# Optimization experiments

Measured on AMD Instinct MI355X. Metric: run time of the kernel, lower is better.

## Reference

```python
import jax, jax.numpy as jnp
import numpy as np

KS = 3
K3 = KS ** 3
NUM_K = 4
KM_ITERS = 10  # fixed Lloyd iterations (original runs to tolerance)


def _unfold3d(xp, d, h, w):
    # xp: [B, C, d+2, h+2, w+2] -> [B, C, d, h, w, 27]; kernel dims flattened as (k1,k2,k3)
    sl = [xp[:, :, i:i + d, j:j + h, l:l + w]
          for i in range(KS) for j in range(KS) for l in range(KS)]
    return jnp.stack(sl, axis=-1)


def _kmeans(pts):
    # pts: [N, C]. Deterministic init with first NUM_K points, fixed Lloyd iterations.
    cent0 = pts[:NUM_K]

    def assign(cent):
        d2 = (jnp.sum(pts * pts, -1, keepdims=True)
              - 2.0 * (pts @ cent.T) + jnp.sum(cent * cent, -1))  # [N, K]
        return jnp.argmin(d2, axis=-1)

    def step(cent, _):
        oh = jax.nn.one_hot(assign(cent), NUM_K, dtype=pts.dtype)  # [N, K]
        cnt = jnp.maximum(oh.sum(0), 1.0)
        cent = (oh.T @ pts) / cnt[:, None]
        return cent, None

    cent, _ = jax.lax.scan(step, cent0, None, length=KM_ITERS)
    return assign(cent), cent


def _mlp3(z, w1, b1, w2, b2, w3, b3):
    z = jax.nn.relu(z @ w1 + b1)
    z = jax.nn.relu(z @ w2 + b2)
    return z @ w3 + b3


def reference(x, proj_w, base_w, gk_w1, gk_b1, gk_w2, gk_b2, gk_w3, gk_b3,
              gb_w1, gb_b1, gb_w2, gb_b2, gb_w3, gb_b3, prelu_a):
    b, c, d, h, w = x.shape
    o = base_w.shape[0]
    n = d * h * w
    x_in = x
    # 1x1x1 input projection (no bias)
    xp = jnp.einsum('oi,bidhw->bodhw', proj_w, x)
    xp = jnp.pad(xp, ((0, 0), (0, 0), (1, 1), (1, 1), (1, 1)))
    patches = _unfold3d(xp, d, h, w)                                # [b,c,d,h,w,27]
    # mean_type 's': mean over kernel dims -> per-voxel channel summary
    x_mean = patches.mean(-1).reshape(b, c, n).transpose(0, 2, 1)   # [b,n,c]
    idx, cent = jax.vmap(_kmeans)(x_mean)                           # [b,n], [b,K,c]
    feat = cent.reshape(b, NUM_K * c)
    # per-cluster dynamic kernel gates in (0,1)
    w_i = jax.nn.sigmoid(_mlp3(feat, gk_w1, gk_b1, gk_w2, gk_b2, gk_w3, gk_b3))
    w_i = w_i.reshape(b, NUM_K, K3).transpose(1, 0, 2)[:, :, None, None, :]  # [K,b,1,1,27]
    weight = (w_i * base_w).reshape(NUM_K, b, o, c * K3)            # [K,b,o,c*27]
    bias = _mlp3(feat, gb_w1, gb_b1, gb_w2, gb_b2, gb_w3, gb_b3)
    bias = bias.reshape(b, NUM_K, o).transpose(1, 0, 2)[..., None]  # [K,b,o,1]
    # im2col: [b, c*27, n] with (c, k) channel-major flattening as in the torch rearrange
    xf = patches.reshape(b, c, n, K3).transpose(0, 1, 3, 2).reshape(b, c * K3, n)
    out = jnp.einsum('kbof,bfn->kbon', weight, xf) + bias           # [K,b,o,n]
    mask = jax.nn.one_hot(idx, NUM_K, dtype=out.dtype)              # [b,n,K]
    out = (out * mask.transpose(2, 0, 1)[:, :, None, :]).sum(0)     # [b,o,n]
    out = out.reshape(b, o, d, h, w)
    out = jnp.where(out >= 0, out, prelu_a * out)                   # PReLU (single param)
    return out + x_in


def setup_inputs():
    key = jax.random.key(0)
    ks = jax.random.split(key, 12)
    B, C, O, D = 1, 64, 64, 40
    inner, inner2 = 128, 64
    fin = C * NUM_K

    def lin(k, i, o_):
        s = 1.0 / np.sqrt(i)
        return jax.random.uniform(k, (i, o_), jnp.float32, -s, s)

    return {
        'x': jax.random.normal(ks[0], (B, C, D, D, D), jnp.float32),
        'proj_w': jax.random.normal(ks[1], (C, C), jnp.float32) / np.sqrt(C),
        'base_w': jax.random.normal(ks[2], (O, C, K3), jnp.float32) / np.sqrt(C * K3),
        'gk_w1': lin(ks[3], fin, inner), 'gk_b1': jnp.zeros((inner,), jnp.float32),
        'gk_w2': lin(ks[4], inner, inner), 'gk_b2': jnp.zeros((inner,), jnp.float32),
        'gk_w3': lin(ks[5], inner, K3 * NUM_K), 'gk_b3': jnp.zeros((K3 * NUM_K,), jnp.float32),
        'gb_w1': lin(ks[6], fin, inner2), 'gb_b1': jnp.zeros((inner2,), jnp.float32),
        'gb_w2': lin(ks[7], inner2, inner2), 'gb_b2': jnp.zeros((inner2,), jnp.float32),
        'gb_w3': lin(ks[8], inner2, O * NUM_K), 'gb_b3': jnp.zeros((O * NUM_K,), jnp.float32),
        'prelu_a': jnp.full((1,), 0.25, jnp.float32),
    }
```

## Files before the change

### kernel.cpp

```cpp
#include <hip/hip_runtime.h>
#include <math.h>

typedef short v8s __attribute__((ext_vector_type(8)));
typedef float v4f __attribute__((ext_vector_type(4)));

#define NVOX 64000
#define NPAD 74088
#define P2   1764
#define GSTR 592704
#define NCPY 32
#define ITST (NCPY*260)

__device__ __forceinline__ unsigned short bf16rne(float f){
  unsigned int u = __float_as_uint(f);
  u += 0x7FFFu + ((u >> 16) & 1u);
  return (unsigned short)(u >> 16);
}

__global__ __launch_bounds__(256) void prep_k(const float* __restrict__ x,
                                              const float* __restrict__ pw,
                                              float* __restrict__ xp,
                                              short* __restrict__ xpt,
                                              const float* __restrict__ bw,
                                              short* __restrict__ bwb){
  int tid = threadIdx.x;
  int bid = blockIdx.x;
  if (bid < 1000){
    int m = (bid >> 2) * 256 + tid;
    int quarter = bid & 3;
    float xv[64];
#pragma unroll
    for (int i = 0; i < 64; i++) xv[i] = x[(size_t)i * NVOX + m];
    int d = m / 1600; int r = m - d * 1600; int h = r / 40; int w = r - h * 40;
    int p = ((d + 1) * 42 + (h + 1)) * 42 + (w + 1);
    const float4* pw4 = (const float4*)pw;
    for (int g8 = quarter * 2; g8 < quarter * 2 + 2; g8++){
      v8s pk;
#pragma unroll
      for (int j = 0; j < 8; j++){
        int co = g8 * 8 + j;
        float acc = 0.f;
#pragma unroll
        for (int q = 0; q < 16; q++){
          float4 pv = pw4[co * 16 + q];
          acc = fmaf(pv.x, xv[4*q+0], acc);
          acc = fmaf(pv.y, xv[4*q+1], acc);
          acc = fmaf(pv.z, xv[4*q+2], acc);
          acc = fmaf(pv.w, xv[4*q+3], acc);
        }
        xp[(size_t)co * NVOX + m] = acc;
        pk[j] = (short)bf16rne(acc);
      }
      *(v8s*)(xpt + (size_t)g8 * GSTR + (size_t)p * 8) = pk;
    }
  } else if (bid < 1432){
    int e = (bid - 1000) * 256 + tid;
    int t5 = e >> 12; int rem = e & 4095;
    int o = rem >> 6; int c = rem & 63;
    bwb[e] = (short)bf16rne(bw[(o * 64 + c) * 27 + t5]);
  } else {
    v8s z = (v8s){0,0,0,0,0,0,0,0};
    for (int p = (bid - 1432) * 256 + tid; p < NPAD; p += 40 * 256){
      int d = p / P2; int rem = p - d * P2; int h = rem / 42; int w = rem - h * 42;
      if (d == 0 || d == 41 || h == 0 || h == 41 || w == 0 || w == 41){
#pragma unroll
        for (int g = 0; g < 8; g++)
          *(v8s*)(xpt + (size_t)g * GSTR + (size_t)p * 8) = z;
      }
    }
  }
}

__global__ __launch_bounds__(256) void boxwh_k(const float* __restrict__ in,
                                               float* __restrict__ out){
  __shared__ float s0[1600], s1[1600];
  size_t base = (size_t)blockIdx.x * 1600;
  int t = threadIdx.x;
  for (int e = t; e < 1600; e += 256) s0[e] = in[base + e];
  __syncthreads();
  for (int e = t; e < 1600; e += 256){
    int w = e % 40;
    float s = s0[e];
    if (w > 0)  s += s0[e - 1];
    if (w < 39) s += s0[e + 1];
    s1[e] = s;
  }
  __syncthreads();
  for (int e = t; e < 1600; e += 256){
    int h = e / 40;
    float s = s1[e];
    if (h > 0)  s += s1[e - 40];
    if (h < 39) s += s1[e + 40];
    out[base + e] = s;
  }
}
__global__ void boxd_k(const float* __restrict__ in, float* __restrict__ out){
  int g = blockIdx.x * 256 + threadIdx.x;
  int d = (g / 1600) % 40;
  float s = in[g];
  if (d > 0)  s += in[g - 1600];
  if (d < 39) s += in[g + 1600];
  out[g] = s * (1.f / 27.f);
}

__global__ __launch_bounds__(256) void transp_k(const float* __restrict__ in,
                                                float* __restrict__ out,
                                                float* __restrict__ km){
  __shared__ float tile[64][65];
  int t = threadIdx.x;
  int nb = blockIdx.x * 64;
  int l = t & 63, g = t >> 6;
  for (int j = 260 + blockIdx.x * 256 + t; j < 11 * ITST; j += 1000 * 256)
    km[j] = 0.f;
  for (int cc = g; cc < 64; cc += 4)
    tile[cc][l] = in[(size_t)cc * NVOX + nb + l];
  __syncthreads();
  if (blockIdx.x == 0){
    km[t] = tile[t & 63][t >> 6];
    if (t < 4) km[256 + t] = 1.f;
  }
  for (int nn = g; nn < 64; nn += 4)
    out[(size_t)(nb + nn) * 64 + l] = tile[l][nn];
}

__global__ __launch_bounds__(256) void assign_k(const float* __restrict__ xmt,
                                                const float* __restrict__ kin,
                                                float* __restrict__ kout,
                                                int* __restrict__ idx, int mode,
                      const float* __restrict__ w1, const float* __restrict__ b1,
                      const float* __restrict__ w2, const float* __restrict__ b2,
                      const float* __restrict__ w3, const float* __restrict__ b3,
                      const float* __restrict__ u1, const float* __restrict__ c1,
                      const float* __restrict__ u2, const float* __restrict__ c2,
                      const float* __restrict__ u3, const float* __restrict__ c3,
                      float* __restrict__ wi, float* __restrict__ bias){
  __shared__ float s_cent[256];
  __shared__ float s_cc[4];
  __shared__ float s_red[260];
  __shared__ float s_x[256 * 65];
  __shared__ int   s_kb[256];
  __shared__ float s_h1[128], s_h2[128], s_g1[64], s_g2[64];
  int t = threadIdx.x, lane = t & 63, wv = t >> 6;
  int n = blockIdx.x * 256 + t;
  {
    float sum = 0.f, cnt = 0.f;
#pragma unroll
    for (int s = 0; s < NCPY; s++){
      sum += kin[s * 260 + t];
      cnt += kin[s * 260 + 256 + (t >> 6)];
    }
    s_cent[t] = sum / fmaxf(cnt, 1.f);
  }
  for (int j = t; j < 260; j += 256) s_red[j] = 0.f;
  __syncthreads();
  if (t < 4){
    const float4* cc4 = (const float4*)(s_cent + t * 64);
    float s = 0.f;
#pragma unroll
    for (int q = 0; q < 16; q++){
      float4 v = cc4[q];
      s = fmaf(v.x, v.x, s); s = fmaf(v.y, v.y, s);
      s = fmaf(v.z, v.z, s); s = fmaf(v.w, v.w, s);
    }
    s_cc[t] = s;
  }
  __syncthreads();
  const float4* xt = (const float4*)(xmt + (size_t)n * 64);
  float4 xq[16];
#pragma unroll
  for (int q = 0; q < 16; q++) xq[q] = xt[q];
  float d0 = 0.f, d1 = 0.f, d2 = 0.f, d3 = 0.f;
  const float4* c4 = (const float4*)s_cent;
#pragma unroll
  for (int q = 0; q < 16; q++){
    float4 p0 = c4[q], p1 = c4[16 + q], p2 = c4[32 + q], p3 = c4[48 + q];
    d0 = fmaf(p0.x, xq[q].x, d0); d0 = fmaf(p0.y, xq[q].y, d0);
    d0 = fmaf(p0.z, xq[q].z, d0); d0 = fmaf(p0.w, xq[q].w, d0);
    d1 = fmaf(p1.x, xq[q].x, d1); d1 = fmaf(p1.y, xq[q].y, d1);
    d1 = fmaf(p1.z, xq[q].z, d1); d1 = fmaf(p1.w, xq[q].w, d1);
    d2 = fmaf(p2.x, xq[q].x, d2); d2 = fmaf(p2.y, xq[q].y, d2);
    d2 = fmaf(p2.z, xq[q].z, d2); d2 = fmaf(p2.w, xq[q].w, d2);
    d3 = fmaf(p3.x, xq[q].x, d3); d3 = fmaf(p3.y, xq[q].y, d3);
    d3 = fmaf(p3.z, xq[q].z, d3); d3 = fmaf(p3.w, xq[q].w, d3);
  }
  float sc0 = s_cc[0] - 2.f * d0;
  float sc1 = s_cc[1] - 2.f * d1;
  float sc2 = s_cc[2] - 2.f * d2;
  float sc3 = s_cc[3] - 2.f * d3;
  int kb = 0; float bs = sc0;
  if (sc1 < bs){ bs = sc1; kb = 1; }
  if (sc2 < bs){ bs = sc2; kb = 2; }
  if (sc3 < bs){ bs = sc3; kb = 3; }
  if (mode){
    idx[n] = kb;
    if (blockIdx.x == 0){
      __syncthreads();
      if (t < 128){
        float z = b1[t];
        for (int i = 0; i < 256; i++) z = fmaf(s_cent[i], w1[i * 128 + t], z);
        s_h1[t] = fmaxf(z, 0.f);
      }
      if (t < 64){
        float z = c1[t];
        for (int i = 0; i < 256; i++) z = fmaf(s_cent[i], u1[i * 64 + t], z);
        s_g1[t] = fmaxf(z, 0.f);
      }
      __syncthreads();
      if (t < 128){
        float z = b2[t];
        for (int i = 0; i < 128; i++) z = fmaf(s_h1[i], w2[i * 128 + t], z);
        s_h2[t] = fmaxf(z, 0.f);
      }
      if (t < 64){
        float z = c2[t];
        for (int i = 0; i < 64; i++) z = fmaf(s_g1[i], u2[i * 64 + t], z);
        s_g2[t] = fmaxf(z, 0.f);
      }
      __syncthreads();
      if (t < 108){
        float z = b3[t];
        for (int i = 0; i < 128; i++) z = fmaf(s_h2[i], w3[i * 108 + t], z);
        wi[t] = 1.f / (1.f + expf(-z));
      }
      {
        float z = c3[t];
        for (int i = 0; i < 64; i++) z = fmaf(s_g2[i], u3[i * 256 + t], z);
        bias[t] = z;
      }
    }
    return;
  }
  s_kb[t] = kb;
#pragma unroll
  for (int q = 0; q < 16; q++){
    s_x[t * 65 + 4*q + 0] = xq[q].x;
    s_x[t * 65 + 4*q + 1] = xq[q].y;
    s_x[t * 65 + 4*q + 2] = xq[q].z;
    s_x[t * 65 + 4*q + 3] = xq[q].w;
  }
  __syncthreads();
  float a0 = 0.f, a1 = 0.f, a2 = 0.f, a3 = 0.f;
  int rowbase = wv * 64;
#pragma unroll 16
  for (int j = 0; j < 64; j++){
    float v = s_x[(rowbase + j) * 65 + lane];
    int kj = s_kb[rowbase + j];
    a0 += (kj == 0) ? v : 0.f;
    a1 += (kj == 1) ? v : 0.f;
    a2 += (kj == 2) ? v : 0.f;
    a3 += (kj == 3) ? v : 0.f;
  }
  atomicAdd(&s_red[lane], a0);
  atomicAdd(&s_red[64 + lane], a1);
  atomicAdd(&s_red[128 + lane], a2);
  atomicAdd(&s_red[192 + lane], a3);
#pragma unroll
  for (int kk = 0; kk < 4; kk++){
    unsigned long long m = __ballot(kb == kk);
    if (lane == 0) atomicAdd(&s_red[256 + kk], (float)__popcll(m));
  }
  __syncthreads();
  float* kslot = kout + (blockIdx.x & (NCPY - 1)) * 260;
  for (int j = t; j < 260; j += 256) atomicAdd(&kslot[j], s_red[j]);
}

__global__ __launch_bounds__(256) void conv_k(const short* __restrict__ xpt,
                                              const short* __restrict__ bwb,
                                              const float* __restrict__ wi,
                                              const float* __restrict__ bias,
                                              const int* __restrict__ idx,
                                              const float* __restrict__ x,
                                              const float* __restrict__ pa,
                                              float* __restrict__ out){
  static const int POFF[27] = {
    -P2-42-1, -P2-42, -P2-42+1, -P2-1, -P2, -P2+1, -P2+42-1, -P2+42, -P2+42+1,
    -42-1, -42, -42+1, -1, 0, 1, 42-1, 42, 42+1,
    P2-42-1, P2-42, P2-42+1, P2-1, P2, P2+1, P2+42-1, P2+42, P2+42+1 };
  __shared__ float s_wi[108];
  __shared__ float s_bias[256];
  __shared__ float s_acc[64 * 68];
  int tid = threadIdx.x;
  for (int j = tid; j < 108; j += 256) s_wi[j] = wi[j];
  s_bias[tid] = bias[tid];
  __syncthreads();
  int wv = tid >> 6, lane = tid & 63;
  int kc = wv & 1, mh = wv >> 1;
  int col = lane & 15, kg = lane >> 4;
  int vb = blockIdx.x * 64;
  int p4[4], ki4[4];
#pragma unroll
  for (int nt = 0; nt < 4; nt++){
    int v = vb + nt * 16 + col;
    ki4[nt] = idx[v];
    int d = v / 1600; int r = v - d * 1600; int h = r / 40; int w = r - h * 40;
    p4[nt] = ((d + 1) * 42 + (h + 1)) * 42 + (w + 1);
  }
  const short* bg = xpt + (size_t)(kc * 4 + kg) * GSTR;
  const short* bp0 = bg + (size_t)p4[0] * 8;
  const short* bp1 = bg + (size_t)p4[1] * 8;
  const short* bp2 = bg + (size_t)p4[2] * 8;
  const short* bp3 = bg + (size_t)p4[3] * 8;
  int ao0 = (mh * 32 + col) * 64 + kc * 32 + kg * 8;
  int ao1 = ao0 + 16 * 64;
  v4f acc[2][4];
#pragma unroll
  for (int m2 = 0; m2 < 2; m2++)
#pragma unroll
    for (int nt = 0; nt < 4; nt++) acc[m2][nt] = (v4f){0.f, 0.f, 0.f, 0.f};
  v4f zero = {0.f, 0.f, 0.f, 0.f};
#pragma unroll 9
  for (int t = 0; t < 27; t++){
    int po8 = POFF[t] * 8;
    v8s a0 = *(const v8s*)(bwb + t * 4096 + ao0);
    v8s a1 = *(const v8s*)(bwb + t * 4096 + ao1);
    v8s b0 = *(const v8s*)(bp0 + po8);
    v8s b1 = *(const v8s*)(bp1 + po8);
    v8s b2 = *(const v8s*)(bp2 + po8);
    v8s b3 = *(const v8s*)(bp3 + po8);
    float wk0 = s_wi[ki4[0] * 27 + t];
    float wk1 = s_wi[ki4[1] * 27 + t];
    float wk2 = s_wi[ki4[2] * 27 + t];
    float wk3 = s_wi[ki4[3] * 27 + t];
    v4f tp;
    tp = __builtin_amdgcn_mfma_f32_16x16x32_bf16(a0, b0, zero, 0, 0, 0); acc[0][0] += tp * wk0;
    tp = __builtin_amdgcn_mfma_f32_16x16x32_bf16(a1, b0, zero, 0, 0, 0); acc[1][0] += tp * wk0;
    tp = __builtin_amdgcn_mfma_f32_16x16x32_bf16(a0, b1, zero, 0, 0, 0); acc[0][1] += tp * wk1;
    tp = __builtin_amdgcn_mfma_f32_16x16x32_bf16(a1, b1, zero, 0, 0, 0); acc[1][1] += tp * wk1;
    tp = __builtin_amdgcn_mfma_f32_16x16x32_bf16(a0, b2, zero, 0, 0, 0); acc[0][2] += tp * wk2;
    tp = __builtin_amdgcn_mfma_f32_16x16x32_bf16(a1, b2, zero, 0, 0, 0); acc[1][2] += tp * wk2;
    tp = __builtin_amdgcn_mfma_f32_16x16x32_bf16(a0, b3, zero, 0, 0, 0); acc[0][3] += tp * wk3;
    tp = __builtin_amdgcn_mfma_f32_16x16x32_bf16(a1, b3, zero, 0, 0, 0); acc[1][3] += tp * wk3;
  }
  __syncthreads();
  if (kc == 1){
#pragma unroll
    for (int m2 = 0; m2 < 2; m2++)
#pragma unroll
      for (int nt = 0; nt < 4; nt++)
        *(v4f*)(&s_acc[(nt * 16 + col) * 68 + mh * 32 + m2 * 16 + kg * 4]) = acc[m2][nt];
  }
  __syncthreads();
  if (kc == 0){
    float pav = pa[0];
#pragma unroll
    for (int m2 = 0; m2 < 2; m2++){
#pragma unroll
      for (int nt = 0; nt < 4; nt++){
        v4f other = *(const v4f*)(&s_acc[(nt * 16 + col) * 68 + mh * 32 + m2 * 16 + kg * 4]);
        v4f sum = acc[m2][nt] + other;
        int n = vb + nt * 16 + col;
#pragma unroll
        for (int r = 0; r < 4; r++){
          int o = mh * 32 + m2 * 16 + kg * 4 + r;
          float val = sum[r] + s_bias[ki4[nt] * 64 + o];
          val = (val >= 0.f) ? val : pav * val;
          size_t off = (size_t)o * NVOX + n;
          out[off] = val + x[off];
        }
      }
    }
  }
}

extern "C" void kernel_launch(void* const* d_in, const int* in_sizes, int n_in,
                              void* d_out, int out_size, void* d_ws, size_t ws_size,
                              hipStream_t stream){
  const float* x    = (const float*)d_in[0];
  const float* pw   = (const float*)d_in[1];
  const float* bw   = (const float*)d_in[2];
  const float* gkw1 = (const float*)d_in[3];
  const float* gkb1 = (const float*)d_in[4];
  const float* gkw2 = (const float*)d_in[5];
  const float* gkb2 = (const float*)d_in[6];
  const float* gkw3 = (const float*)d_in[7];
  const float* gkb3 = (const float*)d_in[8];
  const float* gbw1 = (const float*)d_in[9];
  const float* gbb1 = (const float*)d_in[10];
  const float* gbw2 = (const float*)d_in[11];
  const float* gbb2 = (const float*)d_in[12];
  const float* gbw3 = (const float*)d_in[13];
  const float* gbb3 = (const float*)d_in[14];
  const float* pa   = (const float*)d_in[15];
  float* outp = (float*)d_out;

  float* ws   = (float*)d_ws;
  float* XP   = ws;
  float* BU2  = ws + 4096000;
  float* BU1  = ws + 8192000;
  short* XPT  = (short*)(ws + 12288000);
  short* BWB  = XPT + (size_t)NPAD * 64;
  float* KM   = (float*)(BWB + 110592);
  float* WI   = KM + 11 * ITST;
  float* BIAS = WI + 108;
  int*   IDX  = (int*)(BIAS + 256);
  float* XMT  = XP;

  prep_k<<<1472, 256, 0, stream>>>(x, pw, XP, XPT, bw, BWB);
  boxwh_k<<<2560, 256, 0, stream>>>(XP, BU2);
  boxd_k<<<16000, 256, 0, stream>>>(BU2, BU1);
  transp_k<<<1000, 256, 0, stream>>>(BU1, XMT, KM);
  for (int i = 0; i <= 10; i++)
    assign_k<<<250, 256, 0, stream>>>(XMT, KM + i * ITST, KM + (i + 1) * ITST, IDX,
                                      (i == 10) ? 1 : 0,
                                      gkw1, gkb1, gkw2, gkb2, gkw3, gkb3,
                                      gbw1, gbb1, gbw2, gbb2, gbw3, gbb3,
                                      WI, BIAS);
  conv_k<<<1000, 256, 0, stream>>>(XPT, BWB, WI, BIAS, IDX, x, pa, outp);
}
```

Baseline: 310.1 us.

## Split conv output channels across a second grid dimension to double block count

The conv kernel now launches a 1000x2 grid. Each block handles one 32-channel half of the outputs, and its waves split the 64 voxels into two 16-voxel pairs instead of splitting output channels. Per-thread accumulators shrink from 8 to 4 tiles and the shared reduction buffer shrinks. This raises parallelism and occupancy, at the cost of loading each B (activation) fragment twice across the two blocks and halving the reuse of A fragments.

```diff
diff --git a/kernel.cpp b/kernel.cpp
--- a/kernel.cpp
+++ b/kernel.cpp
@@ -278,35 +278,34 @@
     P2-42-1, P2-42, P2-42+1, P2-1, P2, P2+1, P2+42-1, P2+42, P2+42+1 };
   __shared__ float s_wi[108];
   __shared__ float s_bias[256];
-  __shared__ float s_acc[64 * 68];
+  __shared__ float s_acc[64 * 36];
   int tid = threadIdx.x;
   for (int j = tid; j < 108; j += 256) s_wi[j] = wi[j];
   s_bias[tid] = bias[tid];
   __syncthreads();
   int wv = tid >> 6, lane = tid & 63;
-  int kc = wv & 1, mh = wv >> 1;
+  int kc = wv & 1, nh = wv >> 1;
+  int oh = blockIdx.y;
   int col = lane & 15, kg = lane >> 4;
   int vb = blockIdx.x * 64;
-  int p4[4], ki4[4];
-#pragma unroll
-  for (int nt = 0; nt < 4; nt++){
-    int v = vb + nt * 16 + col;
-    ki4[nt] = idx[v];
+  int p4[2], ki4[2];
+#pragma unroll
+  for (int j = 0; j < 2; j++){
+    int v = vb + (nh * 2 + j) * 16 + col;
+    ki4[j] = idx[v];
     int d = v / 1600; int r = v - d * 1600; int h = r / 40; int w = r - h * 40;
-    p4[nt] = ((d + 1) * 42 + (h + 1)) * 42 + (w + 1);
+    p4[j] = ((d + 1) * 42 + (h + 1)) * 42 + (w + 1);
   }
   const short* bg = xpt + (size_t)(kc * 4 + kg) * GSTR;
   const short* bp0 = bg + (size_t)p4[0] * 8;
   const short* bp1 = bg + (size_t)p4[1] * 8;
-  const short* bp2 = bg + (size_t)p4[2] * 8;
-  const short* bp3 = bg + (size_t)p4[3] * 8;
-  int ao0 = (mh * 32 + col) * 64 + kc * 32 + kg * 8;
+  int ao0 = (oh * 32 + col) * 64 + kc * 32 + kg * 8;
   int ao1 = ao0 + 16 * 64;
-  v4f acc[2][4];
+  v4f acc[2][2];
 #pragma unroll
   for (int m2 = 0; m2 < 2; m2++)
 #pragma unroll
-    for (int nt = 0; nt < 4; nt++) acc[m2][nt] = (v4f){0.f, 0.f, 0.f, 0.f};
+    for (int j = 0; j < 2; j++) acc[m2][j] = (v4f){0.f, 0.f, 0.f, 0.f};
   v4f zero = {0.f, 0.f, 0.f, 0.f};
 #pragma unroll 9
   for (int t = 0; t < 27; t++){
@@ -315,29 +314,21 @@
     v8s a1 = *(const v8s*)(bwb + t * 4096 + ao1);
     v8s b0 = *(const v8s*)(bp0 + po8);
     v8s b1 = *(const v8s*)(bp1 + po8);
-    v8s b2 = *(const v8s*)(bp2 + po8);
-    v8s b3 = *(const v8s*)(bp3 + po8);
     float wk0 = s_wi[ki4[0] * 27 + t];
     float wk1 = s_wi[ki4[1] * 27 + t];
-    float wk2 = s_wi[ki4[2] * 27 + t];
-    float wk3 = s_wi[ki4[3] * 27 + t];
     v4f tp;
     tp = __builtin_amdgcn_mfma_f32_16x16x32_bf16(a0, b0, zero, 0, 0, 0); acc[0][0] += tp * wk0;
     tp = __builtin_amdgcn_mfma_f32_16x16x32_bf16(a1, b0, zero, 0, 0, 0); acc[1][0] += tp * wk0;
     tp = __builtin_amdgcn_mfma_f32_16x16x32_bf16(a0, b1, zero, 0, 0, 0); acc[0][1] += tp * wk1;
     tp = __builtin_amdgcn_mfma_f32_16x16x32_bf16(a1, b1, zero, 0, 0, 0); acc[1][1] += tp * wk1;
-    tp = __builtin_amdgcn_mfma_f32_16x16x32_bf16(a0, b2, zero, 0, 0, 0); acc[0][2] += tp * wk2;
-    tp = __builtin_amdgcn_mfma_f32_16x16x32_bf16(a1, b2, zero, 0, 0, 0); acc[1][2] += tp * wk2;
-    tp = __builtin_amdgcn_mfma_f32_16x16x32_bf16(a0, b3, zero, 0, 0, 0); acc[0][3] += tp * wk3;
-    tp = __builtin_amdgcn_mfma_f32_16x16x32_bf16(a1, b3, zero, 0, 0, 0); acc[1][3] += tp * wk3;
   }
   __syncthreads();
   if (kc == 1){
 #pragma unroll
     for (int m2 = 0; m2 < 2; m2++)
 #pragma unroll
-      for (int nt = 0; nt < 4; nt++)
-        *(v4f*)(&s_acc[(nt * 16 + col) * 68 + mh * 32 + m2 * 16 + kg * 4]) = acc[m2][nt];
+      for (int j = 0; j < 2; j++)
+        *(v4f*)(&s_acc[((nh * 2 + j) * 16 + col) * 36 + m2 * 16 + kg * 4]) = acc[m2][j];
   }
   __syncthreads();
   if (kc == 0){
@@ -345,14 +336,14 @@
 #pragma unroll
     for (int m2 = 0; m2 < 2; m2++){
 #pragma unroll
-      for (int nt = 0; nt < 4; nt++){
-        v4f other = *(const v4f*)(&s_acc[(nt * 16 + col) * 68 + mh * 32 + m2 * 16 + kg * 4]);
-        v4f sum = acc[m2][nt] + other;
-        int n = vb + nt * 16 + col;
+      for (int j = 0; j < 2; j++){
+        v4f other = *(const v4f*)(&s_acc[((nh * 2 + j) * 16 + col) * 36 + m2 * 16 + kg * 4]);
+        v4f sum = acc[m2][j] + other;
+        int n = vb + (nh * 2 + j) * 16 + col;
 #pragma unroll
         for (int r = 0; r < 4; r++){
-          int o = mh * 32 + m2 * 16 + kg * 4 + r;
-          float val = sum[r] + s_bias[ki4[nt] * 64 + o];
+          int o = oh * 32 + m2 * 16 + kg * 4 + r;
+          float val = sum[r] + s_bias[ki4[j] * 64 + o];
           val = (val >= 0.f) ? val : pav * val;
           size_t off = (size_t)o * NVOX + n;
           out[off] = val + x[off];
@@ -405,5 +396,5 @@
                                       gkw1, gkb1, gkw2, gkb2, gkw3, gkb3,
                                       gbw1, gbb1, gbw2, gbb2, gbw3, gbb3,
                                       WI, BIAS);
-  conv_k<<<1000, 256, 0, stream>>>(XPT, BWB, WI, BIAS, IDX, x, pa, outp);
-}
+  conv_k<<<dim3(1000, 2), 256, 0, stream>>>(XPT, BWB, WI, BIAS, IDX, x, pa, outp);
+}
```

After: 348.3 us. +12.3%, slower.

## Fuse depth box-filter, transpose and first k-means assignment; halve conv tile

Applied to the files above, without the earlier changes.

Merges the depth-direction box sum, the transpose kernel and the first Lloyd assignment/accumulation into one kernel that computes the initial centroids directly from the box-filtered input. This removes one intermediate buffer pass and one assign launch. The KM zeroing moves into extra prep_k blocks. The conv kernel now handles 32 voxels per block over 2000 blocks instead of 64 over 1000, trading accumulator reuse of weight loads for more parallelism and lower register pressure. The reduction buffer indexing is reworked so the last assign writes back into slot 0.

```diff
diff --git a/kernel.cpp b/kernel.cpp
--- a/kernel.cpp
+++ b/kernel.cpp
@@ -22,7 +22,8 @@
                                               float* __restrict__ xp,
                                               short* __restrict__ xpt,
                                               const float* __restrict__ bw,
-                                              short* __restrict__ bwb){
+                                              short* __restrict__ bwb,
+                                              float* __restrict__ km){
   int tid = threadIdx.x;
   int bid = blockIdx.x;
   if (bid < 1000){
@@ -58,7 +59,7 @@
     int t5 = e >> 12; int rem = e & 4095;
     int o = rem >> 6; int c = rem & 63;
     bwb[e] = (short)bf16rne(bw[(o * 64 + c) * 27 + t5]);
-  } else {
+  } else if (bid < 1472){
     v8s z = (v8s){0,0,0,0,0,0,0,0};
     for (int p = (bid - 1432) * 256 + tid; p < NPAD; p += 40 * 256){
       int d = p / P2; int rem = p - d * P2; int h = rem / 42; int w = rem - h * 42;
@@ -68,6 +69,9 @@
           *(v8s*)(xpt + (size_t)g * GSTR + (size_t)p * 8) = z;
       }
     }
+  } else {
+    for (int j = (bid - 1472) * 256 + tid; j < 10 * ITST; j += 82 * 256)
+      km[j] = 0.f;
   }
 }
 
@@ -94,31 +98,85 @@
     out[base + e] = s;
   }
 }
-__global__ void boxd_k(const float* __restrict__ in, float* __restrict__ out){
-  int g = blockIdx.x * 256 + threadIdx.x;
-  int d = (g / 1600) % 40;
-  float s = in[g];
-  if (d > 0)  s += in[g - 1600];
-  if (d < 39) s += in[g + 1600];
-  out[g] = s * (1.f / 27.f);
-}
-
-__global__ __launch_bounds__(256) void transp_k(const float* __restrict__ in,
-                                                float* __restrict__ out,
-                                                float* __restrict__ km){
+
+__global__ __launch_bounds__(256) void boxdt_k(const float* __restrict__ in,
+                                               float* __restrict__ out,
+                                               float* __restrict__ acc1){
   __shared__ float tile[64][65];
+  __shared__ float s_cent[256];
+  __shared__ float s_cc[4];
+  __shared__ float s_red[260];
+  __shared__ int   s_kb[64];
   int t = threadIdx.x;
   int nb = blockIdx.x * 64;
   int l = t & 63, g = t >> 6;
-  for (int j = 260 + blockIdx.x * 256 + t; j < 11 * ITST; j += 1000 * 256)
-    km[j] = 0.f;
-  for (int cc = g; cc < 64; cc += 4)
-    tile[cc][l] = in[(size_t)cc * NVOX + nb + l];
-  __syncthreads();
-  if (blockIdx.x == 0){
-    km[t] = tile[t & 63][t >> 6];
-    if (t < 4) km[256 + t] = 1.f;
-  }
+  {
+    int k = t >> 6, c = t & 63;
+    s_cent[t] = (in[(size_t)c * NVOX + k] + in[(size_t)c * NVOX + k + 1600]) * (1.f / 27.f);
+  }
+  for (int j = t; j < 260; j += 256) s_red[j] = 0.f;
+  int n = nb + l;
+  int d = n / 1600;
+  for (int cc = g; cc < 64; cc += 4){
+    const float* b = in + (size_t)cc * NVOX + n;
+    float s = b[0];
+    if (d > 0)  s += b[-1600];
+    if (d < 39) s += b[1600];
+    tile[cc][l] = s * (1.f / 27.f);
+  }
+  __syncthreads();
+  if (t < 4){
+    float s = 0.f;
+    for (int c = 0; c < 64; c++){ float v = s_cent[t * 64 + c]; s = fmaf(v, v, s); }
+    s_cc[t] = s;
+  }
+  __syncthreads();
+  if (t < 64){
+    float d0 = 0.f, d1 = 0.f, d2 = 0.f, d3 = 0.f;
+    for (int c = 0; c < 64; c++){
+      float v = tile[c][t];
+      d0 = fmaf(s_cent[c], v, d0);
+      d1 = fmaf(s_cent[64 + c], v, d1);
+      d2 = fmaf(s_cent[128 + c], v, d2);
+      d3 = fmaf(s_cent[192 + c], v, d3);
+    }
+    float sc0 = s_cc[0] - 2.f * d0;
+    float sc1 = s_cc[1] - 2.f * d1;
+    float sc2 = s_cc[2] - 2.f * d2;
+    float sc3 = s_cc[3] - 2.f * d3;
+    int kb = 0; float bs = sc0;
+    if (sc1 < bs){ bs = sc1; kb = 1; }
+    if (sc2 < bs){ bs = sc2; kb = 2; }
+    if (sc3 < bs){ bs = sc3; kb = 3; }
+    s_kb[t] = kb;
+  }
+  __syncthreads();
+  {
+    int lane = t & 63, wv = t >> 6;
+    float a0 = 0.f, a1 = 0.f, a2 = 0.f, a3 = 0.f;
+#pragma unroll
+    for (int j = 0; j < 16; j++){
+      int p = wv * 16 + j;
+      float v = tile[lane][p];
+      int kj = s_kb[p];
+      a0 += (kj == 0) ? v : 0.f;
+      a1 += (kj == 1) ? v : 0.f;
+      a2 += (kj == 2) ? v : 0.f;
+      a3 += (kj == 3) ? v : 0.f;
+    }
+    atomicAdd(&s_red[lane], a0);
+    atomicAdd(&s_red[64 + lane], a1);
+    atomicAdd(&s_red[128 + lane], a2);
+    atomicAdd(&s_red[192 + lane], a3);
+  }
+  if (t < 4){
+    float c = 0.f;
+    for (int p = 0; p < 64; p++) c += (s_kb[p] == t) ? 1.f : 0.f;
+    s_red[256 + t] = c;
+  }
+  __syncthreads();
+  float* kslot = acc1 + (blockIdx.x & (NCPY - 1)) * 260;
+  for (int j = t; j < 260; j += 256) atomicAdd(&kslot[j], s_red[j]);
   for (int nn = g; nn < 64; nn += 4)
     out[(size_t)(nb + nn) * 64 + l] = tile[l][nn];
 }
@@ -278,7 +336,7 @@
     P2-42-1, P2-42, P2-42+1, P2-1, P2, P2+1, P2+42-1, P2+42, P2+42+1 };
   __shared__ float s_wi[108];
   __shared__ float s_bias[256];
-  __shared__ float s_acc[64 * 68];
+  __shared__ float s_acc[32 * 68];
   int tid = threadIdx.x;
   for (int j = tid; j < 108; j += 256) s_wi[j] = wi[j];
   s_bias[tid] = bias[tid];
@@ -286,10 +344,10 @@
   int wv = tid >> 6, lane = tid & 63;
   int kc = wv & 1, mh = wv >> 1;
   int col = lane & 15, kg = lane >> 4;
-  int vb = blockIdx.x * 64;
-  int p4[4], ki4[4];
-#pragma unroll
-  for (int nt = 0; nt < 4; nt++){
+  int vb = blockIdx.x * 32;
+  int p4[2], ki4[2];
+#pragma unroll
+  for (int nt = 0; nt < 2; nt++){
     int v = vb + nt * 16 + col;
     ki4[nt] = idx[v];
     int d = v / 1600; int r = v - d * 1600; int h = r / 40; int w = r - h * 40;
@@ -298,15 +356,13 @@
   const short* bg = xpt + (size_t)(kc * 4 + kg) * GSTR;
   const short* bp0 = bg + (size_t)p4[0] * 8;
   const short* bp1 = bg + (size_t)p4[1] * 8;
-  const short* bp2 = bg + (size_t)p4[2] * 8;
-  const short* bp3 = bg + (size_t)p4[3] * 8;
   int ao0 = (mh * 32 + col) * 64 + kc * 32 + kg * 8;
   int ao1 = ao0 + 16 * 64;
-  v4f acc[2][4];
+  v4f acc[2][2];
 #pragma unroll
   for (int m2 = 0; m2 < 2; m2++)
 #pragma unroll
-    for (int nt = 0; nt < 4; nt++) acc[m2][nt] = (v4f){0.f, 0.f, 0.f, 0.f};
+    for (int nt = 0; nt < 2; nt++) acc[m2][nt] = (v4f){0.f, 0.f, 0.f, 0.f};
   v4f zero = {0.f, 0.f, 0.f, 0.f};
 #pragma unroll 9
   for (int t = 0; t < 27; t++){
@@ -315,28 +371,20 @@
     v8s a1 = *(const v8s*)(bwb + t * 4096 + ao1);
     v8s b0 = *(const v8s*)(bp0 + po8);
     v8s b1 = *(const v8s*)(bp1 + po8);
-    v8s b2 = *(const v8s*)(bp2 + po8);
-    v8s b3 = *(const v8s*)(bp3 + po8);
     float wk0 = s_wi[ki4[0] * 27 + t];
     float wk1 = s_wi[ki4[1] * 27 + t];
-    float wk2 = s_wi[ki4[2] * 27 + t];
-    float wk3 = s_wi[ki4[3] * 27 + t];
     v4f tp;
     tp = __builtin_amdgcn_mfma_f32_16x16x32_bf16(a0, b0, zero, 0, 0, 0); acc[0][0] += tp * wk0;
     tp = __builtin_amdgcn_mfma_f32_16x16x32_bf16(a1, b0, zero, 0, 0, 0); acc[1][0] += tp * wk0;
     tp = __builtin_amdgcn_mfma_f32_16x16x32_bf16(a0, b1, zero, 0, 0, 0); acc[0][1] += tp * wk1;
     tp = __builtin_amdgcn_mfma_f32_16x16x32_bf16(a1, b1, zero, 0, 0, 0); acc[1][1] += tp * wk1;
-    tp = __builtin_amdgcn_mfma_f32_16x16x32_bf16(a0, b2, zero, 0, 0, 0); acc[0][2] += tp * wk2;
-    tp = __builtin_amdgcn_mfma_f32_16x16x32_bf16(a1, b2, zero, 0, 0, 0); acc[1][2] += tp * wk2;
-    tp = __builtin_amdgcn_mfma_f32_16x16x32_bf16(a0, b3, zero, 0, 0, 0); acc[0][3] += tp * wk3;
-    tp = __builtin_amdgcn_mfma_f32_16x16x32_bf16(a1, b3, zero, 0, 0, 0); acc[1][3] += tp * wk3;
   }
   __syncthreads();
   if (kc == 1){
 #pragma unroll
     for (int m2 = 0; m2 < 2; m2++)
 #pragma unroll
-      for (int nt = 0; nt < 4; nt++)
+      for (int nt = 0; nt < 2; nt++)
         *(v4f*)(&s_acc[(nt * 16 + col) * 68 + mh * 32 + m2 * 16 + kg * 4]) = acc[m2][nt];
   }
   __syncthreads();
@@ -345,7 +393,7 @@
 #pragma unroll
     for (int m2 = 0; m2 < 2; m2++){
 #pragma unroll
-      for (int nt = 0; nt < 4; nt++){
+      for (int nt = 0; nt < 2; nt++){
         v4f other = *(const v4f*)(&s_acc[(nt * 16 + col) * 68 + mh * 32 + m2 * 16 + kg * 4]);
         v4f sum = acc[m2][nt] + other;
         int n = vb + nt * 16 + col;
@@ -386,24 +434,23 @@
   float* ws   = (float*)d_ws;
   float* XP   = ws;
   float* BU2  = ws + 4096000;
-  float* BU1  = ws + 8192000;
   short* XPT  = (short*)(ws + 12288000);
   short* BWB  = XPT + (size_t)NPAD * 64;
   float* KM   = (float*)(BWB + 110592);
-  float* WI   = KM + 11 * ITST;
+  float* WI   = KM + 10 * ITST;
   float* BIAS = WI + 108;
   int*   IDX  = (int*)(BIAS + 256);
   float* XMT  = XP;
 
-  prep_k<<<1472, 256, 0, stream>>>(x, pw, XP, XPT, bw, BWB);
+  prep_k<<<1554, 256, 0, stream>>>(x, pw, XP, XPT, bw, BWB, KM);
   boxwh_k<<<2560, 256, 0, stream>>>(XP, BU2);
-  boxd_k<<<16000, 256, 0, stream>>>(BU2, BU1);
-  transp_k<<<1000, 256, 0, stream>>>(BU1, XMT, KM);
-  for (int i = 0; i <= 10; i++)
-    assign_k<<<250, 256, 0, stream>>>(XMT, KM + i * ITST, KM + (i + 1) * ITST, IDX,
-                                      (i == 10) ? 1 : 0,
+  boxdt_k<<<1000, 256, 0, stream>>>(BU2, XMT, KM);
+  for (int it = 1; it <= 10; it++)
+    assign_k<<<250, 256, 0, stream>>>(XMT, KM + (it - 1) * ITST,
+                                      (it < 10) ? KM + it * ITST : KM, IDX,
+                                      (it == 10) ? 1 : 0,
                                       gkw1, gkb1, gkw2, gkb2, gkw3, gkb3,
                                       gbw1, gbb1, gbw2, gbb2, gbw3, gbb3,
                                       WI, BIAS);
-  conv_k<<<1000, 256, 0, stream>>>(XPT, BWB, WI, BIAS, IDX, x, pa, outp);
-}
+  conv_k<<<2000, 256, 0, stream>>>(XPT, BWB, WI, BIAS, IDX, x, pa, outp);
+}
```

New measurement: 338.2 us. 1.09x slower.
